# Kernel tuning notes

Measured on AMD Instinct MI355X. Metric: run time of the kernel, lower is better.

The kernel has to match this reference:

```python
import jax, jax.numpy as jnp
import numpy as np

BLOCK = 256
EPS = 1e-6

def _silu(x):
    return x * jax.nn.sigmoid(x)

def setup_inputs() -> dict:
    key = jax.random.key(0)
    k1, k2, k3, k4 = jax.random.split(key, 4)
    embed_dim, hidden_dim = 2048, 2048
    b, n, h = 2, 4096, 16
    x = jax.random.normal(k1, (b, n, embed_dim), dtype=jnp.float32)
    slope_rate = jax.random.uniform(k2, (h, 1, 1), dtype=jnp.float32, minval=0.01, maxval=1.0)
    W_qkvu = jax.random.normal(k3, (4 * hidden_dim, embed_dim), dtype=jnp.float32) / np.sqrt(embed_dim)
    W_out = jax.random.normal(k4, (embed_dim, hidden_dim), dtype=jnp.float32) / np.sqrt(hidden_dim)
    return {"x": x, "slope_rate": slope_rate, "W_qkvu": W_qkvu, "W_out": W_out}

def reference(x, slope_rate, W_qkvu, W_out):
    b, n, embed_dim = x.shape
    h = slope_rate.shape[0]
    hidden_dim = W_qkvu.shape[0] // 4
    d = hidden_dim // h  # head dim
    NB = n // BLOCK

    qkvu = x @ W_qkvu.T  # [b, n, 4*hidden]
    q, k, v, u = jnp.split(qkvu, 4, axis=-1)

    def to_heads(t):
        return t.reshape(b, n, h, d).transpose(0, 2, 1, 3)  # b h n d

    q = _silu(to_heads(q))
    k = _silu(to_heads(k))
    v = to_heads(v)

    s = slope_rate  # (h,1,1)
    arr = jnp.arange(1, BLOCK + 1, dtype=x.dtype)  # 1..BLOCK
    q_decay = jnp.exp(-s * arr[:, None])                 # (h, B, 1)
    k_decay = jnp.exp(-s * (BLOCK - arr[:, None]))       # (h, B, 1)
    idx = arr[:, None] - arr[None, :]                    # (B, B)
    diag_decay = jnp.exp(jnp.where(idx >= 0, -s * idx, -jnp.inf))  # (h, B, B)
    block_decay = jnp.exp(-s * BLOCK)                    # (h,1,1)

    # reshape into blocks, scan-major axis first
    def blk(t):
        return t.reshape(b, h, NB, BLOCK, d).transpose(2, 0, 1, 3, 4)

    qb, kb, vb = blk(q), blk(k), blk(v)

    def step(kv, inp):
        qi, ki, vi = inp  # (b,h,B,d)
        qkv_none_diag = jnp.einsum('bhmd,bhde->bhme', qi * q_decay, kv)
        qk = jnp.einsum('bhmd,bhsd->bhms', qi, ki) * diag_decay
        qkv_diag = jnp.einsum('bhms,bhse->bhme', qk, vi)
        kv_new = block_decay * kv + jnp.einsum('bhsd,bhse->bhde', ki * k_decay, vi)
        return kv_new, qkv_none_diag + qkv_diag

    kv0 = jnp.zeros((b, h, d, d), dtype=jnp.float32)
    _, outs = jax.lax.scan(step, kv0, (qb, kb, vb))  # (NB,b,h,B,d)

    o = outs.transpose(1, 2, 0, 3, 4).reshape(b, h, n, d)
    o = o.transpose(0, 2, 1, 3).reshape(b, n, hidden_dim)  # b n (h d)

    # simple RMSNorm (no learned scale)
    o = o * jax.lax.rsqrt(jnp.mean(o * o, axis=-1, keepdims=True) + EPS)
    o = u * o
    return o @ W_out.T
```

## Files before the change

### kernel.cpp

```cpp
#include <hip/hip_runtime.h>
#include <stdint.h>

#define GK 2048

typedef short s16x8 __attribute__((ext_vector_type(8)));
typedef short s16x4 __attribute__((ext_vector_type(4)));
typedef float fx4   __attribute__((ext_vector_type(4)));
typedef unsigned int ux2 __attribute__((ext_vector_type(2)));

#define SB0 __builtin_amdgcn_sched_barrier(0)

__device__ __forceinline__ float b2f(unsigned short s) {
  union { unsigned int u; float f; } x; x.u = ((unsigned int)s) << 16; return x.f;
}
__device__ __forceinline__ unsigned short f2b(float f) {
  union { float f; unsigned int u; } x; x.f = f;
  return (unsigned short)((x.u + 0x7fffu + ((x.u >> 16) & 1u)) >> 16);
}
__device__ __forceinline__ void gl_lds16(const void* g, void* l) {
  __builtin_amdgcn_global_load_lds(
      (const __attribute__((address_space(1))) void*)g,
      (__attribute__((address_space(3))) void*)l, 16, 0, 0);
}

__global__ __launch_bounds__(256, 4) void cvt_bf16(const float* __restrict__ in,
                                                   unsigned short* __restrict__ out) {
  int i = blockIdx.x * 256 + threadIdx.x;
  fx4 v = *(const fx4*)(in + (size_t)i * 4);
  ux2 p;
  p[0] = (unsigned int)f2b(v[0]) | ((unsigned int)f2b(v[1]) << 16);
  p[1] = (unsigned int)f2b(v[2]) | ((unsigned int)f2b(v[3]) << 16);
  *(ux2*)(out + (size_t)i * 4) = p;
}

__global__ void sentinel_k(float* o, float val) { o[threadIdx.x] = val; }

template<int EPI>
__global__ __launch_bounds__(512, 2) void gemm8(
    const unsigned short* __restrict__ A, const unsigned short* __restrict__ B,
    int NT, int nBase,
    unsigned short* __restrict__ qp, unsigned short* __restrict__ kp,
    unsigned short* __restrict__ vp, unsigned short* __restrict__ up,
    float* __restrict__ Cf) {
  __shared__ __align__(16) unsigned short lds8[65536];
  const int nwg = gridDim.x;
  const int bid0 = blockIdx.x;
  const int cpx = nwg >> 3;
  const int bid = (bid0 & 7) * cpx + (bid0 >> 3);
  const int bm = bid / NT, bn = bid % NT;
  const int tid = threadIdx.x;
  const int w = tid >> 6, l = tid & 63;
  const int wr = w >> 2, wc = w & 3;
  const int g = l >> 4, li = l & 15;

  const int srow = l >> 3;
  const int scol = ((l & 7) ^ srow) << 3;
  const unsigned short* Asrc = A + (size_t)(bm * 256) * GK + scol;
  const unsigned short* Bsrc = B + (size_t)(bn * 256) * GK + scol;

  auto stA = [&](int bu, int h, int kt) {
    const unsigned short* s = Asrc + (size_t)(h * 128 + w * 8 + srow) * GK + kt;
    unsigned short* d = &lds8[(bu * 2 + h) * 8192 + w * 512];
    gl_lds16(s, d);
    gl_lds16(s + (size_t)64 * GK, d + 4096);
  };
  auto stB = [&](int bu, int h, int kt) {
    const unsigned short* s = Bsrc + (size_t)(h * 128 + w * 8 + srow) * GK + kt;
    unsigned short* d = &lds8[32768 + (bu * 2 + h) * 8192 + w * 512];
    gl_lds16(s, d);
    gl_lds16(s + (size_t)64 * GK, d + 4096);
  };

  const int s7 = li & 7;
  const int cb0 = ((0 + g) ^ s7) << 3;
  const int cb1 = ((4 + g) ^ s7) << 3;
  const int rbase = li * 64;
  const int Abase0 = wr * 8192;
  const int Bbase0 = 32768 + (wc >> 1) * 8192 + (wc & 1) * 4096;

  s16x8 aF[4][2], bL[2][2], bH[2][2];
  fx4 acc[8][4] = {};

  auto rdA = [&](int rb, int mh) {
    #pragma unroll
    for (int i = 0; i < 4; ++i) {
      int a0 = rb * 16384 + Abase0 + (mh * 4 + i) * 1024 + rbase;
      aF[i][0] = *(const s16x8*)&lds8[a0 + cb0];
      aF[i][1] = *(const s16x8*)&lds8[a0 + cb1];
    }
  };
  auto rdBL = [&](int rb) {
    #pragma unroll
    for (int i = 0; i < 2; ++i) {
      int a0 = rb * 16384 + Bbase0 + i * 1024 + rbase;
      bL[i][0] = *(const s16x8*)&lds8[a0 + cb0];
      bL[i][1] = *(const s16x8*)&lds8[a0 + cb1];
    }
  };
  auto rdBH = [&](int rb) {
    #pragma unroll
    for (int i = 0; i < 2; ++i) {
      int a0 = rb * 16384 + Bbase0 + (2 + i) * 1024 + rbase;
      bH[i][0] = *(const s16x8*)&lds8[a0 + cb0];
      bH[i][1] = *(const s16x8*)&lds8[a0 + cb1];
    }
  };
  auto mm = [&](int mh, int nh, s16x8 (&bF)[2][2]) {
    __builtin_amdgcn_s_setprio(1);
    #pragma unroll
    for (int i = 0; i < 4; ++i)
      #pragma unroll
      for (int j = 0; j < 2; ++j)
        #pragma unroll
        for (int kk = 0; kk < 2; ++kk)
          acc[mh * 4 + i][nh * 2 + j] =
              __builtin_amdgcn_mfma_f32_16x16x32_bf16(aF[i][kk], bF[j][kk],
                                                      acc[mh * 4 + i][nh * 2 + j], 0, 0, 0);
    __builtin_amdgcn_s_setprio(0);
  };

  const int KT = GK / 64;

  stA(0, 0, 0); stB(0, 0, 0); stA(0, 1, 0); stB(0, 1, 0);

  #pragma unroll 2
  for (int t = 0; t < KT - 1; ++t) {
    const int rb = t & 1, wb = rb ^ 1;
    const int ktn = (t + 1) * 64;
    stA(wb, 0, ktn);
    asm volatile("s_waitcnt vmcnt(2)" ::: "memory");
    SB0; __builtin_amdgcn_s_barrier(); SB0;
    rdA(rb, 0); rdBL(rb);
    mm(0, 0, bL);
    SB0; __builtin_amdgcn_s_barrier(); SB0;
    rdBH(rb);
    stB(wb, 0, ktn);
    SB0; __builtin_amdgcn_s_barrier(); SB0;
    mm(0, 1, bH);
    SB0; __builtin_amdgcn_s_barrier(); SB0;
    rdA(rb, 1);
    stA(wb, 1, ktn);
    SB0; __builtin_amdgcn_s_barrier(); SB0;
    mm(1, 1, bH);
    SB0; __builtin_amdgcn_s_barrier(); SB0;
    stB(wb, 1, ktn);
    SB0; __builtin_amdgcn_s_barrier(); SB0;
    mm(1, 0, bL);
    SB0; __builtin_amdgcn_s_barrier(); SB0;
  }
  {
    const int rb = (KT - 1) & 1;
    asm volatile("s_waitcnt vmcnt(0)" ::: "memory");
    SB0; __builtin_amdgcn_s_barrier(); SB0;
    rdA(rb, 0); rdBL(rb);
    mm(0, 0, bL);
    rdBH(rb);
    mm(0, 1, bH);
    rdA(rb, 1);
    mm(1, 1, bH);
    mm(1, 0, bL);
  }

  if (EPI == 0) {
    const int colbase = nBase + bn * 256 + wc * 64;
    #pragma unroll
    for (int mf = 0; mf < 8; ++mf)
      #pragma unroll
      for (int rr = 0; rr < 4; ++rr) {
        int nn = bm * 256 + wr * 128 + mf * 16 + g * 4 + rr;
        #pragma unroll
        for (int nf = 0; nf < 4; ++nf) {
          int colglob = colbase + nf * 16 + li;
          int tq = colglob >> 11, hh = (colglob >> 7) & 15, cl = colglob & 127;
          float vv = acc[mf][nf][rr];
          if (tq < 2) vv = vv / (1.f + __expf(-vv));
          if (tq == 3) up[(size_t)nn * 2048 + hh * 128 + cl] = f2b(vv);
          else ((tq == 0) ? qp : (tq == 1) ? kp : vp)[((size_t)hh * 4096 + nn) * 128 + cl] = f2b(vv);
        }
      }
  } else {
    #pragma unroll
    for (int mf = 0; mf < 8; ++mf)
      #pragma unroll
      for (int rr = 0; rr < 4; ++rr) {
        int row = bm * 256 + wr * 128 + mf * 16 + g * 4 + rr;
        #pragma unroll
        for (int nf = 0; nf < 4; ++nf) {
          int col = bn * 256 + wc * 64 + nf * 16 + li;
          Cf[(size_t)row * 2048 + col] = acc[mf][nf][rr];
        }
      }
  }
}

__global__ __launch_bounds__(256, 2) void gemm_out(
    const unsigned short* __restrict__ A, const unsigned short* __restrict__ B,
    float* __restrict__ Cf) {
  __shared__ __align__(16) short lA[128 * 64];
  __shared__ __align__(16) short lB[128 * 64];
  const int nwg = gridDim.x;
  const int bid0 = blockIdx.x;
  const int cpx = nwg >> 3;
  const int bid = (bid0 & 7) * cpx + (bid0 >> 3);
  const int bm = bid / 16, bn = bid % 16;
  const int tid = threadIdx.x;
  const int w = tid >> 6, l = tid & 63;
  const int wr = w >> 1, wc = w & 1;
  const int g = l >> 4, li = l & 15;

  fx4 acc[4][4] = {};
  const int aRow = l >> 3, aCol = (l & 7) * 8;
  const unsigned short* Abase = A + (size_t)(bm * 128) * GK + aCol;
  const unsigned short* Bbase = B + (size_t)(bn * 128) * GK + aCol;

  for (int kt = 0; kt < GK; kt += 64) {
    __syncthreads();
    #pragma unroll
    for (int j = 0; j < 4; ++j) {
      int c = w * 4 + j;
      gl_lds16(Abase + (size_t)(c * 8 + aRow) * GK + kt, &lA[c * 512]);
      gl_lds16(Bbase + (size_t)(c * 8 + aRow) * GK + kt, &lB[c * 512]);
    }
    __syncthreads();
    #pragma unroll
    for (int kk = 0; kk < 2; ++kk) {
      s16x8 af[4], bf[4];
      #pragma unroll
      for (int mf = 0; mf < 4; ++mf)
        af[mf] = *(const s16x8*)&lA[(wr * 64 + mf * 16 + li) * 64 + kk * 32 + g * 8];
      #pragma unroll
      for (int nf = 0; nf < 4; ++nf)
        bf[nf] = *(const s16x8*)&lB[(wc * 64 + nf * 16 + li) * 64 + kk * 32 + g * 8];
      #pragma unroll
      for (int mf = 0; mf < 4; ++mf)
        #pragma unroll
        for (int nf = 0; nf < 4; ++nf)
          acc[mf][nf] = __builtin_amdgcn_mfma_f32_16x16x32_bf16(af[mf], bf[nf], acc[mf][nf], 0, 0, 0);
    }
  }
  #pragma unroll
  for (int mf = 0; mf < 4; ++mf)
    #pragma unroll
    for (int rr = 0; rr < 4; ++rr) {
      int row = bm * 128 + wr * 64 + mf * 16 + g * 4 + rr;
      #pragma unroll
      for (int nf = 0; nf < 4; ++nf) {
        int col = bn * 128 + wc * 64 + nf * 16 + li;
        Cf[(size_t)row * 2048 + col] = acc[mf][nf][rr];
      }
    }
}

__global__ __launch_bounds__(256, 1) void pass1_C(
    const unsigned short* __restrict__ k, const unsigned short* __restrict__ v,
    const float* __restrict__ slope, float* __restrict__ C) {
  __shared__ __align__(16) unsigned short lK[256 * 128];
  __shared__ __align__(16) unsigned short lV[256 * 128];
  __shared__ float ldecay[256];
  const int bid = blockIdx.x;
  const int h_i = bid >> 4, ib = bid & 15;
  const int tid = threadIdx.x, w = tid >> 6, l = tid & 63;
  const int g = l >> 4, li = l & 15;
  const float r = slope[h_i];
  const size_t kvoff = ((size_t)h_i * 4096 + ib * 256) * 128;
  #pragma unroll
  for (int j = 0; j < 16; ++j) {
    int c = w * 16 + j;
    gl_lds16(k + kvoff + c * 512 + l * 8, &lK[c * 512]);
    gl_lds16(v + kvoff + c * 512 + l * 8, &lV[c * 512]);
  }
  ldecay[tid] = __expf(-r * (float)(255 - tid));
  __syncthreads();

  fx4 acc[2][8] = {};
  #pragma unroll 1
  for (int ks = 0; ks < 8; ++ks) {
    s16x8 a[2], b[8];
    #pragma unroll
    for (int mf = 0; mf < 2; ++mf) {
      int dr = w * 32 + mf * 16 + li;
      #pragma unroll
      for (int e = 0; e < 8; ++e) {
        int s = ks * 32 + g * 8 + e;
        a[mf][e] = (short)f2b(b2f(lK[s * 128 + dr]) * ldecay[s]);
      }
    }
    #pragma unroll
    for (int nf = 0; nf < 8; ++nf) {
      int er = nf * 16 + li;
      #pragma unroll
      for (int e = 0; e < 8; ++e) {
        int s = ks * 32 + g * 8 + e;
        b[nf][e] = (short)lV[s * 128 + er];
      }
    }
    #pragma unroll
    for (int mf = 0; mf < 2; ++mf)
      #pragma unroll
      for (int nf = 0; nf < 8; ++nf)
        acc[mf][nf] = __builtin_amdgcn_mfma_f32_16x16x32_bf16(a[mf], b[nf], acc[mf][nf], 0, 0, 0);
  }
  float* Cb = C + (size_t)bid * 16384;
  #pragma unroll
  for (int mf = 0; mf < 2; ++mf)
    #pragma unroll
    for (int rr = 0; rr < 4; ++rr)
      #pragma unroll
      for (int nf = 0; nf < 8; ++nf)
        Cb[(w * 32 + mf * 16 + g * 4 + rr) * 128 + nf * 16 + li] = acc[mf][nf][rr];
}

__global__ __launch_bounds__(256, 4) void scan_kv2(
    const float* __restrict__ C, const float* __restrict__ slope,
    unsigned short* __restrict__ KVb) {
  __shared__ unsigned short lds[8][128];
  const int h_i = blockIdx.x >> 4, c = blockIdx.x & 15;
  const float r = slope[h_i];
  const float bd = __expf(-256.f * r);
  const int t = threadIdx.x;
  float run[4] = {0.f, 0.f, 0.f, 0.f};
  const int e_out = t >> 1, dg = t & 1;
  for (int i = 0; i < 16; ++i) {
    size_t base = ((size_t)h_i * 16 + i) * 16384;
    fx4 cv = *(const fx4*)(C + base + c * 1024 + t * 4);
    #pragma unroll
    for (int j = 0; j < 4; ++j) lds[t >> 5][(t & 31) * 4 + j] = f2b(run[j]);
    __syncthreads();
    s16x4 ov;
    #pragma unroll
    for (int j = 0; j < 4; ++j) ov[j] = (short)lds[dg * 4 + j][e_out];
    *(s16x4*)&KVb[base + e_out * 128 + c * 8 + dg * 4] = ov;
    __syncthreads();
    #pragma unroll
    for (int j = 0; j < 4; ++j) run[j] = bd * run[j] + cv[j];
  }
}

__global__ __launch_bounds__(256, 1) void pass3_O(
    const unsigned short* __restrict__ q, const unsigned short* __restrict__ k,
    const unsigned short* __restrict__ v, const unsigned short* __restrict__ KVb,
    const float* __restrict__ slope, unsigned short* __restrict__ o) {
  __shared__ __align__(16) unsigned short lK[64 * 128];
  __shared__ __align__(16) unsigned short lV[64 * 128];
  __shared__ __align__(16) unsigned short lP[4 * 64 * 64];
  const int bid = blockIdx.x;
  const int h_i = bid >> 4, ib = bid & 15;
  const int n0 = ib * 256;
  const float r = slope[h_i];
  const int tid = threadIdx.x, w = tid >> 6, l = tid & 63;
  const int g = l >> 4, li = l & 15;
  const int mbase = w * 64;

  fx4 accO[4][8] = {};
  const unsigned short* Qb = q + ((size_t)h_i * 4096 + n0 + mbase) * 128;
  const unsigned short* KVbase = KVb + ((size_t)h_i * 16 + ib) * 16384;

  #pragma unroll
  for (int kd = 0; kd < 4; ++kd) {
    s16x8 aq[4], bkv[8];
    #pragma unroll
    for (int mf = 0; mf < 4; ++mf)
      aq[mf] = *(const s16x8*)(Qb + (size_t)(mf * 16 + li) * 128 + kd * 32 + g * 8);
    #pragma unroll
    for (int nf = 0; nf < 8; ++nf)
      bkv[nf] = *(const s16x8*)(KVbase + (size_t)(nf * 16 + li) * 128 + kd * 32 + g * 8);
    #pragma unroll
    for (int mf = 0; mf < 4; ++mf)
      #pragma unroll
      for (int nf = 0; nf < 8; ++nf)
        accO[mf][nf] = __builtin_amdgcn_mfma_f32_16x16x32_bf16(aq[mf], bkv[nf], accO[mf][nf], 0, 0, 0);
  }
  #pragma unroll
  for (int mf = 0; mf < 4; ++mf)
    #pragma unroll
    for (int rr = 0; rr < 4; ++rr) {
      float f = __expf(-r * (float)(mbase + mf * 16 + g * 4 + rr + 1));
      #pragma unroll
      for (int nf = 0; nf < 8; ++nf) accO[mf][nf][rr] *= f;
    }

  for (int st = 0; st < 4; ++st) {
    __syncthreads();
    #pragma unroll
    for (int j = 0; j < 4; ++j) {
      int c = w * 4 + j;
      size_t roff = ((size_t)h_i * 4096 + n0 + st * 64) * 128 + c * 512 + l * 8;
      gl_lds16(k + roff, &lK[c * 512]);
      gl_lds16(v + roff, &lV[c * 512]);
    }
    __syncthreads();
    if (st > w) continue;

    fx4 sacc[4][4] = {};
    #pragma unroll
    for (int kd = 0; kd < 4; ++kd) {
      s16x8 aq[4], bk[4];
      #pragma unroll
      for (int mf = 0; mf < 4; ++mf)
        aq[mf] = *(const s16x8*)(Qb + (size_t)(mf * 16 + li) * 128 + kd * 32 + g * 8);
      #pragma unroll
      for (int nf = 0; nf < 4; ++nf)
        bk[nf] = *(const s16x8*)&lK[(nf * 16 + li) * 128 + kd * 32 + g * 8];
      #pragma unroll
      for (int mf = 0; mf < 4; ++mf)
        #pragma unroll
        for (int nf = 0; nf < 4; ++nf)
          sacc[mf][nf] = __builtin_amdgcn_mfma_f32_16x16x32_bf16(aq[mf], bk[nf], sacc[mf][nf], 0, 0, 0);
    }

    float f2v[4];
    #pragma unroll
    for (int nf = 0; nf < 4; ++nf) f2v[nf] = __expf(r * (float)(nf * 16 + li));
    unsigned short* lPw = &lP[w * 4096];
    #pragma unroll
    for (int mf = 0; mf < 4; ++mf)
      #pragma unroll
      for (int rr = 0; rr < 4; ++rr) {
        int Aoff = mbase - st * 64 + mf * 16 + g * 4 + rr;
        float f1 = __expf(-r * (float)Aoff);
        #pragma unroll
        for (int nf = 0; nf < 4; ++nf) {
          int sc = nf * 16 + li;
          float val = (Aoff >= sc) ? sacc[mf][nf][rr] * f1 * f2v[nf] : 0.f;
          lPw[(mf * 16 + g * 4 + rr) * 64 + sc] = f2b(val);
        }
      }

    #pragma unroll
    for (int ks = 0; ks < 2; ++ks) {
      s16x8 pa[4], vb[8];
      #pragma unroll
      for (int mf = 0; mf < 4; ++mf)
        pa[mf] = *(const s16x8*)&lPw[(mf * 16 + li) * 64 + ks * 32 + g * 8];
      #pragma unroll
      for (int nf = 0; nf < 8; ++nf) {
        int er = nf * 16 + li;
        #pragma unroll
        for (int e = 0; e < 8; ++e) {
          int s = ks * 32 + g * 8 + e;
          vb[nf][e] = (short)lV[s * 128 + er];
        }
      }
      #pragma unroll
      for (int mf = 0; mf < 4; ++mf)
        #pragma unroll
        for (int nf = 0; nf < 8; ++nf)
          accO[mf][nf] = __builtin_amdgcn_mfma_f32_16x16x32_bf16(pa[mf], vb[nf], accO[mf][nf], 0, 0, 0);
    }
  }

  #pragma unroll
  for (int mf = 0; mf < 4; ++mf)
    #pragma unroll
    for (int rr = 0; rr < 4; ++rr) {
      int nn = n0 + mbase + mf * 16 + g * 4 + rr;
      unsigned short* ob = o + (size_t)nn * 2048 + h_i * 128;
      #pragma unroll
      for (int nf = 0; nf < 8; ++nf)
        ob[nf * 16 + li] = f2b(accO[mf][nf][rr]);
    }
}

__global__ __launch_bounds__(256, 4) void norm_mul(
    const unsigned short* __restrict__ o, const unsigned short* __restrict__ u,
    unsigned short* __restrict__ z) {
  __shared__ float red[4];
  const int row = blockIdx.x, t = threadIdx.x;
  const size_t base = (size_t)row * 2048 + t * 8;
  s16x8 ov = *(const s16x8*)(o + base);
  float vals[8]; float ss = 0.f;
  #pragma unroll
  for (int j = 0; j < 8; ++j) { vals[j] = b2f((unsigned short)ov[j]); ss += vals[j] * vals[j]; }
  #pragma unroll
  for (int dl = 1; dl < 64; dl <<= 1) ss += __shfl_xor(ss, dl);
  if ((t & 63) == 0) red[t >> 6] = ss;
  __syncthreads();
  float tot = red[0] + red[1] + red[2] + red[3];
  float rs = rsqrtf(tot * (1.f / 2048.f) + 1e-6f);
  s16x8 uv = *(const s16x8*)(u + base);
  s16x8 zv;
  #pragma unroll
  for (int j = 0; j < 8; ++j)
    zv[j] = (short)f2b(vals[j] * b2f((unsigned short)uv[j]) * rs);
  *(s16x8*)(z + base) = zv;
}

extern "C" void kernel_launch(void* const* d_in, const int* in_sizes, int n_in,
                              void* d_out, int out_size, void* d_ws, size_t ws_size,
                              hipStream_t stream) {
  (void)in_sizes; (void)n_in; (void)out_size;
  const float* x     = (const float*)d_in[0];
  const float* slope = (const float*)d_in[1];
  const float* Wqkvu = (const float*)d_in[2];
  const float* Wout  = (const float*)d_in[3];
  float* out = (float*)d_out;

  const size_t NEED_MED  = 92274688ull;
  const size_t NEED_BIG  = 125829120ull;
  const size_t NEED_HUGE = 167772160ull;
  if (ws_size < NEED_MED) {
    sentinel_k<<<1, 256, 0, stream>>>(out, (float)((double)ws_size * 1e-6));
    return;
  }
  char* ws = (char*)d_ws;

  if (ws_size >= NEED_HUGE) {
    unsigned short* wq  = (unsigned short*)(ws + 0);
    unsigned short* xz  = (unsigned short*)(ws + 33554432);
    unsigned short* qb  = (unsigned short*)(ws + 67108864);
    unsigned short* kb  = (unsigned short*)(ws + 83886080);
    unsigned short* vb  = (unsigned short*)(ws + 100663296);
    unsigned short* ub  = (unsigned short*)(ws + 117440512);
    unsigned short* S0  = (unsigned short*)(ws + 134217728);
    unsigned short* KVr = (unsigned short*)(ws + 150994944);
    cvt_bf16<<<16384, 256, 0, stream>>>(Wqkvu, wq);
    cvt_bf16<<<16384, 256, 0, stream>>>(x, xz);
    for (int bb = 0; bb < 2; ++bb) {
      unsigned short* xzb = xz + (size_t)bb * 8388608;
      gemm8<0><<<512, 512, 0, stream>>>(xzb, wq, 32, 0, qb, kb, vb, ub, nullptr);
      pass1_C<<<256, 256, 0, stream>>>(kb, vb, slope, (float*)S0);
      scan_kv2<<<256, 256, 0, stream>>>((float*)S0, slope, KVr);
      pass3_O<<<256, 256, 0, stream>>>(qb, kb, vb, KVr, slope, S0);
      norm_mul<<<4096, 256, 0, stream>>>(S0, ub, xzb);
    }
    cvt_bf16<<<4096, 256, 0, stream>>>(Wout, KVr);
    gemm8<1><<<256, 512, 0, stream>>>(xz, KVr, 8, 0,
                                      nullptr, nullptr, nullptr, nullptr, out);
  } else if (ws_size >= NEED_BIG) {
    unsigned short* wq  = (unsigned short*)(ws + 0);
    unsigned short* S0  = (unsigned short*)(ws + 33554432);
    unsigned short* qb  = (unsigned short*)(ws + 50331648);
    unsigned short* kb  = (unsigned short*)(ws + 67108864);
    unsigned short* vb  = (unsigned short*)(ws + 83886080);
    unsigned short* ub  = (unsigned short*)(ws + 100663296);
    unsigned short* KVr = (unsigned short*)(ws + 117440512);
    cvt_bf16<<<16384, 256, 0, stream>>>(Wqkvu, wq);
    for (int bb = 0; bb < 2; ++bb) {
      const float* xB = x + (size_t)bb * 8388608;
      float* outB = out + (size_t)bb * 8388608;
      cvt_bf16<<<8192, 256, 0, stream>>>(xB, S0);
      gemm8<0><<<512, 512, 0, stream>>>(S0, wq, 32, 0, qb, kb, vb, ub, nullptr);
      pass1_C<<<256, 256, 0, stream>>>(kb, vb, slope, (float*)S0);
      scan_kv2<<<256, 256, 0, stream>>>((float*)S0, slope, KVr);
      pass3_O<<<256, 256, 0, stream>>>(qb, kb, vb, KVr, slope, S0);
      cvt_bf16<<<4096, 256, 0, stream>>>(Wout, KVr);
      norm_mul<<<4096, 256, 0, stream>>>(S0, ub, qb);
      gemm_out<<<512, 256, 0, stream>>>(qb, KVr, outB);
    }
  } else {
    unsigned short* reg0 = (unsigned short*)(ws + 0);
    unsigned short* qb   = (unsigned short*)(ws + 16777216);
    unsigned short* kb   = (unsigned short*)(ws + 33554432);
    unsigned short* vb   = (unsigned short*)(ws + 50331648);
    unsigned short* ub   = (unsigned short*)(ws + 67108864);
    unsigned short* KVr  = (unsigned short*)(ws + 83886080);
    for (int bb = 0; bb < 2; ++bb) {
      const float* xB = x + (size_t)bb * 8388608;
      float* outB = out + (size_t)bb * 8388608;
      cvt_bf16<<<8192, 256, 0, stream>>>(xB, reg0);
      cvt_bf16<<<8192, 256, 0, stream>>>(Wqkvu, vb);
      gemm8<0><<<256, 512, 0, stream>>>(reg0, vb, 16, 0, qb, kb, vb, ub, nullptr);
      cvt_bf16<<<4096, 256, 0, stream>>>(Wqkvu + 8388608, KVr);
      gemm8<0><<<128, 512, 0, stream>>>(reg0, KVr, 8, 4096, qb, kb, vb, ub, nullptr);
      cvt_bf16<<<4096, 256, 0, stream>>>(Wqkvu + 12582912, KVr);
      gemm8<0><<<128, 512, 0, stream>>>(reg0, KVr, 8, 6144, qb, kb, vb, ub, nullptr);
      pass1_C<<<256, 256, 0, stream>>>(kb, vb, slope, (float*)reg0);
      scan_kv2<<<256, 256, 0, stream>>>((float*)reg0, slope, KVr);
      pass3_O<<<256, 256, 0, stream>>>(qb, kb, vb, KVr, slope, reg0);
      norm_mul<<<4096, 256, 0, stream>>>(reg0, ub, qb);
      cvt_bf16<<<4096, 256, 0, stream>>>(Wout, reg0);
      gemm_out<<<512, 256, 0, stream>>>(qb, reg0, outB);
    }
  }
}
```

Baseline: 515.8 us.

## Run QKVU projection as one GEMM over both batches and fuse bf16 conversions

Adds a workspace tier in which the QKVU projection runs once over both batches as a single 1024-workgroup GEMM. A new epilogue mode splits rows by batch and writes per-batch q/k/v/u buffers. The two fp32-to-bf16 conversion launches are merged into one kernel that picks its source by thread index. The aim is fewer launches and a fuller GPU during the big GEMM, at the cost of roughly double the q/k/v/u workspace. The new path only runs if the harness workspace reaches the larger threshold.

```diff
diff --git a/kernel.cpp b/kernel.cpp
--- a/kernel.cpp
+++ b/kernel.cpp
@@ -31,6 +31,20 @@
   p[0] = (unsigned int)f2b(v[0]) | ((unsigned int)f2b(v[1]) << 16);
   p[1] = (unsigned int)f2b(v[2]) | ((unsigned int)f2b(v[3]) << 16);
   *(ux2*)(out + (size_t)i * 4) = p;
+}
+
+__global__ __launch_bounds__(256, 4) void cvt2_bf16(
+    const float* __restrict__ a, unsigned short* __restrict__ oa, int na4,
+    const float* __restrict__ b, unsigned short* __restrict__ ob) {
+  int i = blockIdx.x * 256 + threadIdx.x;
+  const float* src; unsigned short* dst; int j;
+  if (i < na4) { src = a; dst = oa; j = i; }
+  else         { src = b; dst = ob; j = i - na4; }
+  fx4 v = *(const fx4*)(src + (size_t)j * 4);
+  ux2 p;
+  p[0] = (unsigned int)f2b(v[0]) | ((unsigned int)f2b(v[1]) << 16);
+  p[1] = (unsigned int)f2b(v[2]) | ((unsigned int)f2b(v[3]) << 16);
+  *(ux2*)(dst + (size_t)j * 4) = p;
 }
 
 __global__ void sentinel_k(float* o, float val) { o[threadIdx.x] = val; }
@@ -161,21 +175,24 @@
     mm(1, 0, bL);
   }
 
-  if (EPI == 0) {
+  if (EPI == 0 || EPI == 2) {
     const int colbase = nBase + bn * 256 + wc * 64;
     #pragma unroll
     for (int mf = 0; mf < 8; ++mf)
       #pragma unroll
       for (int rr = 0; rr < 4; ++rr) {
-        int nn = bm * 256 + wr * 128 + mf * 16 + g * 4 + rr;
+        int row = bm * 256 + wr * 128 + mf * 16 + g * 4 + rr;
+        int nn = row, bb = 0;
+        if (EPI == 2) { bb = row >> 12; nn = row & 4095; }
+        size_t boff = (size_t)bb * 8388608;
         #pragma unroll
         for (int nf = 0; nf < 4; ++nf) {
           int colglob = colbase + nf * 16 + li;
           int tq = colglob >> 11, hh = (colglob >> 7) & 15, cl = colglob & 127;
           float vv = acc[mf][nf][rr];
           if (tq < 2) vv = vv / (1.f + __expf(-vv));
-          if (tq == 3) up[(size_t)nn * 2048 + hh * 128 + cl] = f2b(vv);
-          else ((tq == 0) ? qp : (tq == 1) ? kp : vp)[((size_t)hh * 4096 + nn) * 128 + cl] = f2b(vv);
+          if (tq == 3) up[boff + (size_t)nn * 2048 + hh * 128 + cl] = f2b(vv);
+          else ((tq == 0) ? qp : (tq == 1) ? kp : vp)[boff + ((size_t)hh * 4096 + nn) * 128 + cl] = f2b(vv);
         }
       }
   } else {
@@ -495,16 +512,38 @@
   const float* Wout  = (const float*)d_in[3];
   float* out = (float*)d_out;
 
-  const size_t NEED_MED  = 92274688ull;
-  const size_t NEED_BIG  = 125829120ull;
-  const size_t NEED_HUGE = 167772160ull;
+  const size_t NEED_MED   = 92274688ull;
+  const size_t NEED_BIG   = 125829120ull;
+  const size_t NEED_HUGE  = 167772160ull;
+  const size_t NEED_GIANT = 226492416ull;
   if (ws_size < NEED_MED) {
     sentinel_k<<<1, 256, 0, stream>>>(out, (float)((double)ws_size * 1e-6));
     return;
   }
   char* ws = (char*)d_ws;
 
-  if (ws_size >= NEED_HUGE) {
+  if (ws_size >= NEED_GIANT) {
+    unsigned short* wq  = (unsigned short*)(ws + 0);
+    unsigned short* xz  = (unsigned short*)(ws + 33554432);
+    unsigned short* qb  = (unsigned short*)(ws + 67108864);
+    unsigned short* kb  = (unsigned short*)(ws + 100663296);
+    unsigned short* vb  = (unsigned short*)(ws + 134217728);
+    unsigned short* ub  = (unsigned short*)(ws + 167772160);
+    unsigned short* S0  = (unsigned short*)(ws + 201326592);
+    unsigned short* KVr = (unsigned short*)(ws + 218103808);
+    cvt2_bf16<<<32768, 256, 0, stream>>>(Wqkvu, wq, 4194304, x, xz);
+    gemm8<2><<<1024, 512, 0, stream>>>(xz, wq, 32, 0, qb, kb, vb, ub, nullptr);
+    for (int bb = 0; bb < 2; ++bb) {
+      size_t boff = (size_t)bb * 8388608;
+      pass1_C<<<256, 256, 0, stream>>>(kb + boff, vb + boff, slope, (float*)S0);
+      scan_kv2<<<256, 256, 0, stream>>>((float*)S0, slope, KVr);
+      pass3_O<<<256, 256, 0, stream>>>(qb + boff, kb + boff, vb + boff, KVr, slope, S0);
+      norm_mul<<<4096, 256, 0, stream>>>(S0, ub + boff, xz + boff);
+    }
+    cvt_bf16<<<4096, 256, 0, stream>>>(Wout, KVr);
+    gemm8<1><<<256, 512, 0, stream>>>(xz, KVr, 8, 0,
+                                      nullptr, nullptr, nullptr, nullptr, out);
+  } else if (ws_size >= NEED_HUGE) {
     unsigned short* wq  = (unsigned short*)(ws + 0);
     unsigned short* xz  = (unsigned short*)(ws + 33554432);
     unsigned short* qb  = (unsigned short*)(ws + 67108864);
@@ -513,8 +552,7 @@
     unsigned short* ub  = (unsigned short*)(ws + 117440512);
     unsigned short* S0  = (unsigned short*)(ws + 134217728);
     unsigned short* KVr = (unsigned short*)(ws + 150994944);
-    cvt_bf16<<<16384, 256, 0, stream>>>(Wqkvu, wq);
-    cvt_bf16<<<16384, 256, 0, stream>>>(x, xz);
+    cvt2_bf16<<<32768, 256, 0, stream>>>(Wqkvu, wq, 4194304, x, xz);
     for (int bb = 0; bb < 2; ++bb) {
       unsigned short* xzb = xz + (size_t)bb * 8388608;
       gemm8<0><<<512, 512, 0, stream>>>(xzb, wq, 32, 0, qb, kb, vb, ub, nullptr);
```

Result: no change. 508.4 us (-1.4%).
